# Performance work log

Hardware: AMD Instinct MI355X
Metric: run time of the kernel (lower is better)

The kernel has to match this reference:

```python
import jax, jax.numpy as jnp
import numpy as np

N = 131072      # total nodes
G = 1024        # graphs
NPG = 128       # nodes per graph (equal-sized graphs, batch sorted)
E = 2097152     # edges (avg degree 16)
H = 64          # hidden_channels
K = 30          # sort-pool k
MAXZ = 1000     # max_z
D = 3 * H + 1   # total_latent_dim = hidden*num_layers + 1 = 193
DENSE = ((K - 2) // 2 + 1 - 5 + 1) * 32  # 352


def setup_inputs():
    key = jax.random.key(0)
    ks = jax.random.split(key, 16)
    z = jax.random.randint(ks[0], (N,), 0, MAXZ)
    # within-graph random edges
    g = jax.random.randint(ks[1], (E,), 0, G)
    src = g * NPG + jax.random.randint(ks[2], (E,), 0, NPG)
    dst = g * NPG + jax.random.randint(ks[3], (E,), 0, NPG)
    edge_index = jnp.stack([src, dst])
    batch = jnp.repeat(jnp.arange(G), NPG)

    def w(k, shape, fan):
        return jax.random.normal(k, shape, dtype=jnp.float32) / np.float32(np.sqrt(fan))

    z_table = w(ks[4], (MAXZ, H), H)
    W0 = w(ks[5], (H, H), H); b0 = jnp.zeros((H,), jnp.float32)
    W1 = w(ks[6], (H, H), H); b1 = jnp.zeros((H,), jnp.float32)
    W2 = w(ks[7], (H, H), H); b2 = jnp.zeros((H,), jnp.float32)
    W3 = w(ks[8], (H, 1), H); b3 = jnp.zeros((1,), jnp.float32)
    conv1_w = w(ks[9], (16, D), D); conv1_b = jnp.zeros((16,), jnp.float32)
    conv2_w = w(ks[10], (32, 16, 5), 16 * 5); conv2_b = jnp.zeros((32,), jnp.float32)
    lin1_w = w(ks[11], (DENSE, 128), DENSE); lin1_b = jnp.zeros((128,), jnp.float32)
    lin2_w = w(ks[12], (128, 1), 128); lin2_b = jnp.zeros((1,), jnp.float32)
    return dict(z=z, edge_index=edge_index, batch=batch, z_table=z_table,
                W0=W0, b0=b0, W1=W1, b1=b1, W2=W2, b2=b2, W3=W3, b3=b3,
                conv1_w=conv1_w, conv1_b=conv1_b, conv2_w=conv2_w, conv2_b=conv2_b,
                lin1_w=lin1_w, lin1_b=lin1_b, lin2_w=lin2_w, lin2_b=lin2_b)


def _forward(z, edge_index, z_table, W0, b0, W1, b1, W2, b2, W3, b3,
             conv1_w, conv1_b, conv2_w, conv2_b, lin1_w, lin1_b, lin2_w, lin2_b):
    src, dst = edge_index[0], edge_index[1]
    loop = jnp.arange(N)
    src_sl = jnp.concatenate([src, loop])  # self-loops (gcn_norm)
    dst_sl = jnp.concatenate([dst, loop])
    deg = jax.ops.segment_sum(jnp.ones((E + N,), jnp.float32), dst_sl, num_segments=N)
    dinv = jnp.where(deg > 0, 1.0 / jnp.sqrt(deg), 0.0)
    norm = dinv[src_sl] * dinv[dst_sl]  # sym-normalized edge weights

    def gcn(x, W, b):
        h = x @ W
        agg = jax.ops.segment_sum(h[src_sl] * norm[:, None], dst_sl, num_segments=N)
        return agg + b

    x = z_table[z]  # z_embedding lookup, [N, H]
    xs = []
    for W, b in ((W0, b0), (W1, b1), (W2, b2), (W3, b3)):
        x = jnp.tanh(gcn(x, W, b))
        xs.append(x)
    xc = jnp.concatenate(xs, axis=-1)  # [N, D] (concat of xs[1:])

    # global_sort_pool: sort per graph by last channel (descending), keep top-K.
    xg = xc.reshape(G, NPG, D)
    order = jnp.argsort(-xg[:, :, -1], axis=1)[:, :K]
    topk = jnp.take_along_axis(xg, order[:, :, None], axis=1)  # [G, K, D]

    # conv1: kernel=stride=D over flattened [G, 1, K*D] == per-node linear D->16
    h1 = jax.nn.relu(jnp.einsum('gkd,cd->gck', topk, conv1_w) + conv1_b[None, :, None])  # [G,16,K]
    p = h1.reshape(G, 16, K // 2, 2).max(-1)  # maxpool1d(2,2) -> [G,16,15]
    h2 = jax.nn.relu(
        jax.lax.conv_general_dilated(p, conv2_w, (1,), 'VALID',
                                     dimension_numbers=('NCH', 'OIH', 'NCH'))
        + conv2_b[None, :, None])  # [G,32,11]
    flat = h2.reshape(G, -1)  # channel-major flatten, matches torch .view
    hm = jax.nn.relu(flat @ lin1_w + lin1_b)  # MLP (dropout off in eval)
    return hm @ lin2_w + lin2_b  # [G, 1]


def reference(z, edge_index, batch, z_table, W0, b0, W1, b1, W2, b2, W3, b3,
              conv1_w, conv1_b, conv2_w, conv2_b, lin1_w, lin1_b, lin2_w, lin2_b):
    del batch  # graphs are equal-sized & node ids contiguous: reshape implements sort-pool segmentation
    return _forward(z, edge_index, z_table, W0, b0, W1, b1, W2, b2, W3, b3,
                    conv1_w, conv1_b, conv2_w, conv2_b, lin1_w, lin1_b, lin2_w, lin2_b)
```

## Files before the change

### kernel.cpp

```cpp
#include <hip/hip_runtime.h>

#define NGRAPH  1024
#define E_EDGES 2097152
#define ECAP    2944
#define MAXZ    1000

__device__ __forceinline__ float bfu_lo(unsigned u) { return __uint_as_float(u << 16); }
__device__ __forceinline__ float bfu_hi(unsigned u) { return __uint_as_float(u & 0xFFFF0000u); }
__device__ __forceinline__ unsigned packlo(float f0, float f1) {
    return (__float_as_uint(f0) >> 16) | (__float_as_uint(f1) & 0xFFFF0000u);
}
__device__ __forceinline__ int xh_idx(int r, int k)  { return (r << 6) | (k  ^ ((r & 7) << 3)); }
__device__ __forceinline__ int xl_idx(int r, int k2) { return (r << 5) | (k2 ^ ((r & 7) << 2)); }

__device__ __forceinline__ double tanh_fast(double p) {
    double q = 2.0 * p;
    q = fmin(40.0, fmax(-40.0, q));
    double nf = rint(q * 1.4426950408889634074);
    double r  = fma(nf, -6.93147180369123816490e-01, q);
    r = fma(nf, -1.90821492927058770002e-10, r);
    double er =     2.755731922398589e-07;
    er = fma(er, r, 2.755731922398589e-06);
    er = fma(er, r, 2.4801587301587302e-05);
    er = fma(er, r, 1.984126984126984e-04);
    er = fma(er, r, 1.3888888888888889e-03);
    er = fma(er, r, 8.333333333333333e-03);
    er = fma(er, r, 4.1666666666666664e-02);
    er = fma(er, r, 1.6666666666666666e-01);
    er = fma(er, r, 0.5);
    er = fma(er, r, 1.0);
    er = fma(er, r, 1.0);
    double E = er * __longlong_as_double((long long)(1023 + (int)nf) << 52);
    return 1.0 - 2.0 / (E + 1.0);
}

__global__ void markWS_kernel(float* out) {
    int i = blockIdx.x * 256 + threadIdx.x;
    if (i < NGRAPH) out[i] = 2.0f;
}

__global__ void adjscatter_kernel(const int* __restrict__ ei,
                                  unsigned* __restrict__ adjG) {
    int e = blockIdx.x * 256 + threadIdx.x;
    if (e >= E_EDGES) return;
    int s = ei[e];
    int d = ei[E_EDGES + e];
    int g = s >> 7;
    int sl = s & 127, dl = d & 127;
    atomicAdd(&adjG[((size_t)g << 12) + (dl << 5) + (sl >> 2)], 1u << ((sl & 3) << 3));
}

__global__ __launch_bounds__(1024, 1) void gnn2_kernel(
    const int* __restrict__ z,
    const unsigned* __restrict__ adjG,
    const float* __restrict__ zt,
    const float* __restrict__ W0, const float* __restrict__ b0,
    const float* __restrict__ W1, const float* __restrict__ b1,
    const float* __restrict__ W2, const float* __restrict__ b2,
    const float* __restrict__ W3, const float* __restrict__ b3,
    const float* __restrict__ c1w, const float* __restrict__ c1b,
    const float* __restrict__ c2w, const float* __restrict__ c2b,
    const float* __restrict__ l1w, const float* __restrict__ l1b,
    const float* __restrict__ l2w, const float* __restrict__ l2b,
    float* __restrict__ xdump,
    float* __restrict__ out)
{
    __shared__ __align__(16) float    Xhi[2][8192];
    __shared__ __align__(16) unsigned Xlo[2][4096];
    __shared__ unsigned char  csr[2][ECAP];
    __shared__ unsigned short rp16[2][132];
    __shared__ int            aux[2][128];
    __shared__ int            inv[2][30];
    __shared__ float          kd30f[2][30];
    __shared__ int            w0tot[2];

    const int half = threadIdx.x >> 9;
    const int tt   = threadIdx.x & 511;
    const int g    = (blockIdx.x << 1) | half;
    const int r0 = tt >> 3;
    const int r1 = r0 + 64;
    const int c0 = (tt & 7) << 3;

    float*          XH = Xhi[half];
    unsigned*       XL = Xlo[half];
    unsigned char*  CS = csr[half];
    unsigned short* RP = rp16[half];
    int*            AX = aux[half];

    unsigned* adjM = (unsigned*)XH;

    {
        const uint4* src = (const uint4*)(adjG + ((size_t)g << 12));
        uint4* dst = (uint4*)adjM;
        for (int i = tt; i < 1024; i += 512) dst[i] = src[i];
    }
    if (tt < 30) { inv[half][tt] = tt; kd30f[half][tt] = 0.f; }
    __syncthreads();

    int degv = 0;
    if (tt < 128) {
        for (int w = 0; w < 32; ++w) {
            unsigned u = adjM[(tt << 5) + w];
            degv += (int)((u & 255u) + ((u >> 8) & 255u) + ((u >> 16) & 255u) + (u >> 24));
        }
        AX[tt] = degv;
    }
    if (tt < 128) {
        int v = degv;
        for (int o = 1; o < 64; o <<= 1) {
            int u = __shfl_up(v, o, 64);
            if ((tt & 63) >= o) v += u;
        }
        if (tt == 63) w0tot[half] = v;
        RP[tt + 1] = (unsigned short)v;
    }
    __syncthreads();
    if (tt >= 64 && tt < 128) RP[tt + 1] = (unsigned short)(RP[tt + 1] + w0tot[half]);
    if (tt == 0) RP[0] = 0;
    __syncthreads();

    const int mydeg = (tt < 128) ? AX[tt] : 0;
    const double dv0 = 1.0 / sqrt((double)(AX[r0] + 1));
    const double dv1 = 1.0 / sqrt((double)(AX[r1] + 1));
    const double dvm = 1.0 / sqrt((double)(mydeg + 1));

    if (tt < 128) {
        unsigned pos = RP[tt];
        for (int w = 0; w < 32; ++w) {
            unsigned u = adjM[(tt << 5) + w];
            while (u) {
                int b2 = (u & 0xFFu) ? 0 : (u & 0xFF00u) ? 1 : (u & 0xFF0000u) ? 2 : 3;
                int m = (int)((u >> (b2 << 3)) & 255u);
                unsigned char sv = (unsigned char)((w << 2) + b2);
                for (int q = 0; q < m; ++q) { if (pos < ECAP) CS[pos] = sv; ++pos; }
                u &= ~(0xFFu << (b2 << 3));
            }
        }
    }
    __syncthreads();

    for (int idx = tt; idx < 8192; idx += 512) {
        int n = idx >> 6, c = idx & 63;
        int zv = z[(g << 7) + n];
        zv = (zv < 0) ? 0 : ((zv >= MAXZ) ? MAXZ - 1 : zv);
        XH[xh_idx(n, c)] = zt[zv * 64 + c];
    }
    __syncthreads();

    for (int layer = 0; layer < 3; ++layer) {
        const float* Wg = (layer == 0) ? W0 : (layer == 1) ? W1 : W2;
        const float* bg = (layer == 0) ? b0 : (layer == 1) ? b1 : b2;
        const bool haslo = (layer != 0);

        double accd0[8], accd1[8]; float accf0[8], accf1[8];
#pragma unroll
        for (int j = 0; j < 8; ++j) { accd0[j] = 0.0; accd1[j] = 0.0; accf0[j] = 0.f; accf1[j] = 0.f; }

        for (int k = 0; k < 64; k += 4) {
            float4 a0 = *(const float4*)&XH[xh_idx(r0, k)];
            float4 a1 = *(const float4*)&XH[xh_idx(r1, k)];
            float x0[4] = {a0.x, a0.y, a0.z, a0.w};
            float x1[4] = {a1.x, a1.y, a1.z, a1.w};
            float l0[4], l1[4];
            if (haslo) {
                uint2 u0 = *(const uint2*)&XL[xl_idx(r0, k >> 1)];
                uint2 u1 = *(const uint2*)&XL[xl_idx(r1, k >> 1)];
                l0[0] = bfu_lo(u0.x); l0[1] = bfu_hi(u0.x); l0[2] = bfu_lo(u0.y); l0[3] = bfu_hi(u0.y);
                l1[0] = bfu_lo(u1.x); l1[1] = bfu_hi(u1.x); l1[2] = bfu_lo(u1.y); l1[3] = bfu_hi(u1.y);
            }
#pragma unroll
            for (int kk = 0; kk < 4; ++kk) {
                const float* wr = Wg + ((k + kk) << 6) + c0;
                float4 wa = *(const float4*)wr;
                float4 wb = *(const float4*)(wr + 4);
                float wf[8] = {wa.x, wa.y, wa.z, wa.w, wb.x, wb.y, wb.z, wb.w};
                double xd0 = (double)x0[kk], xd1 = (double)x1[kk];
#pragma unroll
                for (int j = 0; j < 8; ++j) {
                    double wd = (double)wf[j];
                    accd0[j] = fma(xd0, wd, accd0[j]);
                    accd1[j] = fma(xd1, wd, accd1[j]);
                }
                if (haslo) {
#pragma unroll
                    for (int j = 0; j < 8; ++j) {
                        accf0[j] = fmaf(l0[kk], wf[j], accf0[j]);
                        accf1[j] = fmaf(l1[kk], wf[j], accf1[j]);
                    }
                }
            }
        }
        __syncthreads();

        float hfv[2][8], rsv[2][8];
#pragma unroll
        for (int rw = 0; rw < 2; ++rw) {
            int rr = rw ? r1 : r0;
            double dv = rw ? dv1 : dv0;
#pragma unroll
            for (int j = 0; j < 8; ++j) {
                double acc = rw ? (accd1[j] + (double)accf1[j]) : (accd0[j] + (double)accf0[j]);
                double h = dv * acc;
                float hf = (float)h;
                hfv[rw][j] = hf;
                rsv[rw][j] = (float)(h - (double)hf);
            }
            int bi = xh_idx(rr, c0);
            *(float4*)&XH[bi]     = make_float4(hfv[rw][0], hfv[rw][1], hfv[rw][2], hfv[rw][3]);
            *(float4*)&XH[bi + 4] = make_float4(hfv[rw][4], hfv[rw][5], hfv[rw][6], hfv[rw][7]);
            uint4 lv;
            lv.x = packlo(rsv[rw][0], rsv[rw][1]);
            lv.y = packlo(rsv[rw][2], rsv[rw][3]);
            lv.z = packlo(rsv[rw][4], rsv[rw][5]);
            lv.w = packlo(rsv[rw][6], rsv[rw][7]);
            *(uint4*)&XL[xl_idx(rr, c0 >> 1)] = lv;
        }
        __syncthreads();

        double ad[2][8]; float af[2][8];
#pragma unroll
        for (int rw = 0; rw < 2; ++rw)
#pragma unroll
            for (int j = 0; j < 8; ++j) { ad[rw][j] = (double)hfv[rw][j]; af[rw][j] = rsv[rw][j]; }

#pragma unroll
        for (int rw = 0; rw < 2; ++rw) {
            int rr = rw ? r1 : r0;
            for (unsigned e = RP[rr]; e < RP[rr + 1]; ++e) {
                int s = CS[e];
                int bi = (s << 6) | (c0 ^ ((s & 7) << 3));
                float4 a = *(const float4*)&XH[bi];
                float4 b = *(const float4*)&XH[bi + 4];
                uint4 lu = *(const uint4*)&XL[(s << 5) | ((c0 >> 1) ^ ((s & 7) << 2))];
                ad[rw][0] += (double)a.x; ad[rw][1] += (double)a.y;
                ad[rw][2] += (double)a.z; ad[rw][3] += (double)a.w;
                ad[rw][4] += (double)b.x; ad[rw][5] += (double)b.y;
                ad[rw][6] += (double)b.z; ad[rw][7] += (double)b.w;
                af[rw][0] += bfu_lo(lu.x); af[rw][1] += bfu_hi(lu.x);
                af[rw][2] += bfu_lo(lu.y); af[rw][3] += bfu_hi(lu.y);
                af[rw][4] += bfu_lo(lu.z); af[rw][5] += bfu_hi(lu.z);
                af[rw][6] += bfu_lo(lu.w); af[rw][7] += bfu_hi(lu.w);
            }
        }
        __syncthreads();

#pragma unroll
        for (int rw = 0; rw < 2; ++rw) {
            int rr = rw ? r1 : r0;
            double dv = rw ? dv1 : dv0;
            float vf[8], rs[8];
#pragma unroll
            for (int j = 0; j < 8; ++j) {
                double v = tanh_fast(dv * (ad[rw][j] + (double)af[rw][j]) + (double)bg[c0 + j]);
                float vfl = (float)v;
                vf[j] = vfl;
                rs[j] = (float)(v - (double)vfl);
            }
            int bi = xh_idx(rr, c0);
            *(float4*)&XH[bi]     = make_float4(vf[0], vf[1], vf[2], vf[3]);
            *(float4*)&XH[bi + 4] = make_float4(vf[4], vf[5], vf[6], vf[7]);
            uint4 lv;
            lv.x = packlo(rs[0], rs[1]);
            lv.y = packlo(rs[2], rs[3]);
            lv.z = packlo(rs[4], rs[5]);
            lv.w = packlo(rs[6], rs[7]);
            *(uint4*)&XL[xl_idx(rr, c0 >> 1)] = lv;

            if (layer < 2) {
                float* xd = xdump + (((size_t)g * 2 + layer) << 13) + (rr << 6) + c0;
                *(float4*)xd       = make_float4(vf[0], vf[1], vf[2], vf[3]);
                *(float4*)(xd + 4) = make_float4(vf[4], vf[5], vf[6], vf[7]);
            }
        }
        __syncthreads();
    }

    double* h4sD  = (double*)XL;
    double* keydD = ((double*)XL) + 128;

    double sdreg = 0.0;
    if (tt < 128) {
        double sd = 0.0; float sf = 0.f;
        for (int k = 0; k < 64; k += 4) {
            float4 a = *(const float4*)&XH[xh_idx(tt, k)];
            uint2  u = *(const uint2*)&XL[xl_idx(tt, k >> 1)];
            float4 w = *(const float4*)&W3[k];
            sd = fma((double)a.x, (double)w.x, sd);
            sd = fma((double)a.y, (double)w.y, sd);
            sd = fma((double)a.z, (double)w.z, sd);
            sd = fma((double)a.w, (double)w.w, sd);
            sf = fmaf(bfu_lo(u.x), w.x, sf);
            sf = fmaf(bfu_hi(u.x), w.y, sf);
            sf = fmaf(bfu_lo(u.y), w.z, sf);
            sf = fmaf(bfu_hi(u.y), w.w, sf);
        }
        sdreg = sd + (double)sf;
    }
    __syncthreads();
    if (tt < 128) h4sD[tt] = dvm * sdreg;
    __syncthreads();
    double keyreg = 0.0;
    if (tt < 128) {
        double a = h4sD[tt];
        for (unsigned e = RP[tt]; e < RP[tt + 1]; ++e) a += h4sD[CS[e]];
        keyreg = tanh_fast(dvm * a + (double)b3[0]);
        keydD[tt] = keyreg;
    }
    __syncthreads();

    if (tt < 128) {
        int rk = 0;
        for (int j = 0; j < 128; ++j) {
            double kj = keydD[j];
            if (kj > keyreg || (kj == keyreg && j < tt)) ++rk;
        }
        if (rk < 30) { inv[half][rk] = tt; kd30f[half][rk] = (float)keyreg; }
    }
    __syncthreads();

    float* XloF = (float*)XL;
    float* h1v = XloF + 2560;
    float* ppv = XloF + 3040;
    float* flv = XloF + 3280;
    float* hmv = XloF + 3632;

    if (tt < 480) {
        int c = tt & 15, k = tt >> 4;
        int node = inv[half][k];
        const float* wrow = c1w + c * 193;
        const float* xg0 = xdump + ((size_t)g * 2) * 8192 + node * 64;
        const float* xg1 = xg0 + 8192;
        float s8[8];
#pragma unroll
        for (int cg = 0; cg < 8; ++cg) {
            float acc = 0.f;
            float4 xa = *(const float4*)&xg0[cg * 8];
            float4 xb = *(const float4*)&xg0[cg * 8 + 4];
            const float* w0p = wrow + cg * 8;
            acc = fmaf(xa.x, w0p[0], acc); acc = fmaf(xa.y, w0p[1], acc);
            acc = fmaf(xa.z, w0p[2], acc); acc = fmaf(xa.w, w0p[3], acc);
            acc = fmaf(xb.x, w0p[4], acc); acc = fmaf(xb.y, w0p[5], acc);
            acc = fmaf(xb.z, w0p[6], acc); acc = fmaf(xb.w, w0p[7], acc);
            float4 ya = *(const float4*)&xg1[cg * 8];
            float4 yb = *(const float4*)&xg1[cg * 8 + 4];
            const float* w1p = wrow + 64 + cg * 8;
            acc = fmaf(ya.x, w1p[0], acc); acc = fmaf(ya.y, w1p[1], acc);
            acc = fmaf(ya.z, w1p[2], acc); acc = fmaf(ya.w, w1p[3], acc);
            acc = fmaf(yb.x, w1p[4], acc); acc = fmaf(yb.y, w1p[5], acc);
            acc = fmaf(yb.z, w1p[6], acc); acc = fmaf(yb.w, w1p[7], acc);
            const float* w2p = wrow + 128 + cg * 8;
#pragma unroll
            for (int j = 0; j < 8; ++j)
                acc = fmaf(XH[xh_idx(node, cg * 8 + j)], w2p[j], acc);
            s8[cg] = acc;
        }
        float A0 = s8[0] + s8[1], A1 = s8[2] + s8[3];
        float A2 = s8[4] + s8[5], A3 = s8[6] + s8[7];
        float G = (A0 + A1) + (A2 + A3);
        float s = G + c1w[c * 193 + 192] * kd30f[half][k] + c1b[c];
        h1v[c * 30 + k] = s > 0.f ? s : 0.f;
    }
    __syncthreads();
    if (tt < 240) {
        int c = tt & 15, i = tt >> 4;
        float a = h1v[c * 30 + 2 * i], b = h1v[c * 30 + 2 * i + 1];
        ppv[c * 15 + i] = a > b ? a : b;
    }
    __syncthreads();
    if (tt < 352) {
        int o = tt / 11, j = tt % 11;
        float s = c2b[o];
        for (int i = 0; i < 16; ++i)
#pragma unroll
            for (int u = 0; u < 5; ++u)
                s = fmaf(ppv[i * 15 + j + u], c2w[o * 80 + i * 5 + u], s);
        flv[tt] = s > 0.f ? s : 0.f;
    }
    __syncthreads();
    if (tt < 128) {
        float s = l1b[tt];
        for (int i = 0; i < 352; ++i) s = fmaf(flv[i], l1w[i * 128 + tt], s);
        hmv[tt] = s > 0.f ? s : 0.f;
    }
    __syncthreads();
    if (tt < 64) {
        float v = fmaf(hmv[tt], l2w[tt], hmv[tt + 64] * l2w[tt + 64]);
#pragma unroll
        for (int o = 32; o > 0; o >>= 1) v += __shfl_down(v, o, 64);
        if (tt == 0) out[g] = v + l2b[0];
    }
}

__global__ __launch_bounds__(512, 2) void gnn_kernel(
    const int* __restrict__ z,
    const unsigned* __restrict__ adjG,
    const float* __restrict__ zt,
    const float* __restrict__ W0, const float* __restrict__ b0,
    const float* __restrict__ W1, const float* __restrict__ b1,
    const float* __restrict__ W2, const float* __restrict__ b2,
    const float* __restrict__ W3, const float* __restrict__ b3,
    const float* __restrict__ c1w, const float* __restrict__ c1b,
    const float* __restrict__ c2w, const float* __restrict__ c2b,
    const float* __restrict__ l1w, const float* __restrict__ l1b,
    const float* __restrict__ l2w, const float* __restrict__ l2b,
    float* __restrict__ out)
{
    __shared__ __align__(16) float    Xhi[8192];
    __shared__ __align__(16) unsigned Xlo[4096];
    __shared__ unsigned char  csr[ECAP];
    __shared__ unsigned short rp16[132];
    __shared__ int            aux[128];
    __shared__ int            inv[30];
    __shared__ float          kd30f[30];
    __shared__ int            w0tot;

    const int g  = blockIdx.x;
    const int t  = threadIdx.x;
    const int r0 = t >> 3;
    const int r1 = r0 + 64;
    const int c0 = (t & 7) << 3;

    unsigned* adjM = (unsigned*)Xhi;

    {
        const uint4* src = (const uint4*)(adjG + ((size_t)g << 12));
        uint4* dst = (uint4*)adjM;
        for (int i = t; i < 1024; i += 512) dst[i] = src[i];
    }
    if (t < 30) { inv[t] = t; kd30f[t] = 0.f; }
    __syncthreads();

    int degv = 0;
    if (t < 128) {
        for (int w = 0; w < 32; ++w) {
            unsigned u = adjM[(t << 5) + w];
            degv += (int)((u & 255u) + ((u >> 8) & 255u) + ((u >> 16) & 255u) + (u >> 24));
        }
        aux[t] = degv;
    }
    if (t < 128) {
        int v = degv;
        for (int o = 1; o < 64; o <<= 1) {
            int u = __shfl_up(v, o, 64);
            if ((t & 63) >= o) v += u;
        }
        if (t == 63) w0tot = v;
        rp16[t + 1] = (unsigned short)v;
    }
    __syncthreads();
    if (t >= 64 && t < 128) rp16[t + 1] = (unsigned short)(rp16[t + 1] + w0tot);
    if (t == 0) rp16[0] = 0;
    __syncthreads();

    const int mydeg = (t < 128) ? aux[t] : 0;
    const double dv0 = 1.0 / sqrt((double)(aux[r0] + 1));
    const double dv1 = 1.0 / sqrt((double)(aux[r1] + 1));
    const double dvm = 1.0 / sqrt((double)(mydeg + 1));

    if (t < 128) {
        unsigned pos = rp16[t];
        for (int w = 0; w < 32; ++w) {
            unsigned u = adjM[(t << 5) + w];
            while (u) {
                int b2 = (u & 0xFFu) ? 0 : (u & 0xFF00u) ? 1 : (u & 0xFF0000u) ? 2 : 3;
                int m = (int)((u >> (b2 << 3)) & 255u);
                unsigned char sv = (unsigned char)((w << 2) + b2);
                for (int q = 0; q < m; ++q) { if (pos < ECAP) csr[pos] = sv; ++pos; }
                u &= ~(0xFFu << (b2 << 3));
            }
        }
    }
    __syncthreads();

// ... 122 lines not shown
            }
            int bi = xh_idx(rr, c0);
            *(float4*)&Xhi[bi]     = make_float4(vf[0], vf[1], vf[2], vf[3]);
            *(float4*)&Xhi[bi + 4] = make_float4(vf[4], vf[5], vf[6], vf[7]);
            uint4 lv;
            lv.x = packlo(rs[0], rs[1]);
            lv.y = packlo(rs[2], rs[3]);
            lv.z = packlo(rs[4], rs[5]);
            lv.w = packlo(rs[6], rs[7]);
            *(uint4*)&Xlo[xl_idx(rr, c0 >> 1)] = lv;

            const float* w1base = c1w + layer * 64 + c0;
            for (int c = 0; c < 16; ++c) {
                const float* wr = w1base + c * 193;
#pragma unroll
                for (int j = 0; j < 8; ++j)
                    g1p[rw][c] = fmaf(vf[j], wr[j], g1p[rw][c]);
            }
        }
        __syncthreads();
    }

    double* h4sD  = (double*)Xlo;
    double* keydD = ((double*)Xlo) + 128;

    double sdreg = 0.0;
    if (t < 128) {
        double sd = 0.0; float sf = 0.f;
        for (int k = 0; k < 64; k += 4) {
            float4 a = *(const float4*)&Xhi[xh_idx(t, k)];
            uint2  u = *(const uint2*)&Xlo[xl_idx(t, k >> 1)];
            float4 w = *(const float4*)&W3[k];
            sd = fma((double)a.x, (double)w.x, sd);
            sd = fma((double)a.y, (double)w.y, sd);
            sd = fma((double)a.z, (double)w.z, sd);
            sd = fma((double)a.w, (double)w.w, sd);
            sf = fmaf(bfu_lo(u.x), w.x, sf);
            sf = fmaf(bfu_hi(u.x), w.y, sf);
            sf = fmaf(bfu_lo(u.y), w.z, sf);
            sf = fmaf(bfu_hi(u.y), w.w, sf);
        }
        sdreg = sd + (double)sf;
    }
    __syncthreads();
    if (t < 128) h4sD[t] = dvm * sdreg;
    __syncthreads();
    double keyreg = 0.0;
    if (t < 128) {
        double a = h4sD[t];
        for (unsigned e = rp16[t]; e < rp16[t + 1]; ++e) a += h4sD[csr[e]];
        keyreg = tanh_fast(dvm * a + (double)b3[0]);
        keydD[t] = keyreg;
    }
    __syncthreads();

    if (t < 128) {
        int rk = 0;
        for (int j = 0; j < 128; ++j) {
            double kj = keydD[j];
            if (kj > keyreg || (kj == keyreg && j < t)) ++rk;
        }
        if (rk < 30) { inv[rk] = t; kd30f[rk] = (float)keyreg; }
    }

#pragma unroll
    for (int m = 1; m <= 4; m <<= 1) {
#pragma unroll
        for (int rw = 0; rw < 2; ++rw)
#pragma unroll
            for (int c = 0; c < 16; ++c)
                g1p[rw][c] += __shfl_xor(g1p[rw][c], m, 64);
    }
    __syncthreads();
    float* XloF = (float*)Xlo;
    float* G1   = XloF + 512;
    if ((t & 7) == 0) {
#pragma unroll
        for (int c = 0; c < 16; c += 4) {
            *(float4*)&G1[r0 * 16 + c] = make_float4(g1p[0][c], g1p[0][c + 1], g1p[0][c + 2], g1p[0][c + 3]);
            *(float4*)&G1[r1 * 16 + c] = make_float4(g1p[1][c], g1p[1][c + 1], g1p[1][c + 2], g1p[1][c + 3]);
        }
    }
    __syncthreads();

    float* h1v = XloF + 2560;
    float* ppv = XloF + 3040;
    float* flv = XloF + 3280;
    float* hmv = XloF + 3632;

    if (t < 480) {
        int c = t & 15, k = t >> 4;
        int node = inv[k];
        float s = G1[node * 16 + c] + c1w[c * 193 + 192] * kd30f[k] + c1b[c];
        h1v[c * 30 + k] = s > 0.f ? s : 0.f;
    }
    __syncthreads();
    if (t < 240) {
        int c = t & 15, i = t >> 4;
        float a = h1v[c * 30 + 2 * i], b = h1v[c * 30 + 2 * i + 1];
        ppv[c * 15 + i] = a > b ? a : b;
    }
    __syncthreads();
    if (t < 352) {
        int o = t / 11, j = t % 11;
        float s = c2b[o];
        for (int i = 0; i < 16; ++i)
#pragma unroll
            for (int u = 0; u < 5; ++u)
                s = fmaf(ppv[i * 15 + j + u], c2w[o * 80 + i * 5 + u], s);
        flv[t] = s > 0.f ? s : 0.f;
    }
    __syncthreads();
    if (t < 128) {
        float s = l1b[t];
        for (int i = 0; i < 352; ++i) s = fmaf(flv[i], l1w[i * 128 + t], s);
        hmv[t] = s > 0.f ? s : 0.f;
    }
    __syncthreads();
    if (t < 64) {
        float v = fmaf(hmv[t], l2w[t], hmv[t + 64] * l2w[t + 64]);
#pragma unroll
        for (int o = 32; o > 0; o >>= 1) v += __shfl_down(v, o, 64);
        if (t == 0) out[g] = v + l2b[0];
    }
}


extern "C" void kernel_launch(void* const* d_in, const int* in_sizes, int n_in,
                              void* d_out, int out_size, void* d_ws, size_t ws_size,
                              hipStream_t stream) {
    const int*   z   = (const int*)d_in[0];
    const int*   ei  = (const int*)d_in[1];
    const float* zt  = (const float*)d_in[3];
    const float* W0  = (const float*)d_in[4];
    const float* b0  = (const float*)d_in[5];
    const float* W1  = (const float*)d_in[6];
    const float* b1  = (const float*)d_in[7];
    const float* W2  = (const float*)d_in[8];
    const float* b2  = (const float*)d_in[9];
    const float* W3  = (const float*)d_in[10];
    const float* b3  = (const float*)d_in[11];
    const float* c1w = (const float*)d_in[12];
    const float* c1b = (const float*)d_in[13];
    const float* c2w = (const float*)d_in[14];
    const float* c2b = (const float*)d_in[15];
    const float* l1w = (const float*)d_in[16];
    const float* l1b = (const float*)d_in[17];
    const float* l2w = (const float*)d_in[18];
    const float* l2b = (const float*)d_in[19];
    float* out = (float*)d_out;

    const size_t ADJ_B = (size_t)NGRAPH * 4096 * 4;
    const size_t XD_B  = (size_t)NGRAPH * 2 * 8192 * 4;
    if (ws_size < ADJ_B) {
        markWS_kernel<<<4, 256, 0, stream>>>(out);
        return;
    }

    unsigned* adjG = (unsigned*)d_ws;

    hipMemsetAsync(adjG, 0, ADJ_B, stream);
    adjscatter_kernel<<<(E_EDGES + 255) / 256, 256, 0, stream>>>(ei, adjG);

    if (ws_size >= ADJ_B + XD_B) {
        float* xdump = (float*)((char*)d_ws + ADJ_B);
        gnn2_kernel<<<NGRAPH / 2, 1024, 0, stream>>>(z, adjG, zt,
                                                     W0, b0, W1, b1, W2, b2, W3, b3,
                                                     c1w, c1b, c2w, c2b, l1w, l1b, l2w, l2b,
                                                     xdump, out);
    } else {
        gnn_kernel<<<NGRAPH, 512, 0, stream>>>(z, adjG, zt,
                                               W0, b0, W1, b1, W2, b2, W3, b3,
                                               c1w, c1b, c2w, c2b, l1w, l1b, l2w, l2b,
                                               out);
    }
}
```

Measured before the change: 599.7 us.

## Use FP64 MFMA for per-layer dense transform with runtime correctness probe

```diff
diff --git a/kernel.cpp b/kernel.cpp
--- a/kernel.cpp
+++ b/kernel.cpp
@@ -4,6 +4,17 @@
 #define E_EDGES 2097152
 #define ECAP    2944
 #define MAXZ    1000
+
+#if defined(__has_builtin)
+#  if __has_builtin(__builtin_amdgcn_mfma_f64_16x16x4f64)
+#    define HAVE_MFMA64 1
+#  endif
+#endif
+#ifndef HAVE_MFMA64
+#  define HAVE_MFMA64 0
+#endif
+
+typedef __attribute__((ext_vector_type(4))) double double4v;
 
 __device__ __forceinline__ float bfu_lo(unsigned u) { return __uint_as_float(u << 16); }
 __device__ __forceinline__ float bfu_hi(unsigned u) { return __uint_as_float(u & 0xFFFF0000u); }
@@ -50,6 +61,32 @@
     atomicAdd(&adjG[((size_t)g << 12) + (dl << 5) + (sl >> 2)], 1u << ((sl & 3) << 3));
 }
 
+__global__ void mfmaprobe_kernel(int* flag) {
+#if HAVE_MFMA64
+    int l = threadIdx.x;
+    int i16 = l & 15, kq = l >> 4;
+    double A = (double)(i16 * 17 + kq * 3 + 1);
+    double B = (double)(kq * 7 + i16 * 29 + 2);
+    double4v acc = {0.0, 0.0, 0.0, 0.0};
+    acc = __builtin_amdgcn_mfma_f64_16x16x4f64(A, B, acc, 0, 0, 0);
+    bool ok = true;
+#pragma unroll
+    for (int v = 0; v < 4; ++v) {
+        int i = (kq << 2) + v;
+        int j = i16;
+        double ref = 0.0;
+#pragma unroll
+        for (int k = 0; k < 4; ++k)
+            ref += (double)(i * 17 + k * 3 + 1) * (double)(k * 7 + j * 29 + 2);
+        ok = ok && (acc[v] == ref);
+    }
+    unsigned long long m = __ballot(ok);
+    if (l == 0) flag[0] = (m == 0xFFFFFFFFFFFFFFFFull) ? 1 : 0;
+#else
+    if (threadIdx.x == 0) flag[0] = 0;
+#endif
+}
+
 __global__ __launch_bounds__(1024, 1) void gnn2_kernel(
     const int* __restrict__ z,
     const unsigned* __restrict__ adjG,
@@ -62,6 +99,7 @@
     const float* __restrict__ c2w, const float* __restrict__ c2b,
     const float* __restrict__ l1w, const float* __restrict__ l1b,
     const float* __restrict__ l2w, const float* __restrict__ l2b,
+    const int* __restrict__ mfmaflag,
     float* __restrict__ xdump,
     float* __restrict__ out)
 {
@@ -87,6 +125,10 @@
     unsigned short* RP = rp16[half];
     int*            AX = aux[half];
 
+#if HAVE_MFMA64
+    const bool use_mfma = (mfmaflag[0] != 0);
+#endif
+
     unsigned* adjM = (unsigned*)XH;
 
     {
@@ -152,124 +194,247 @@
         const float* bg = (layer == 0) ? b0 : (layer == 1) ? b1 : b2;
         const bool haslo = (layer != 0);
 
-        double accd0[8], accd1[8]; float accf0[8], accf1[8];
-#pragma unroll
-        for (int j = 0; j < 8; ++j) { accd0[j] = 0.0; accd1[j] = 0.0; accf0[j] = 0.f; accf1[j] = 0.f; }
-
-        for (int k = 0; k < 64; k += 4) {
-            float4 a0 = *(const float4*)&XH[xh_idx(r0, k)];
-            float4 a1 = *(const float4*)&XH[xh_idx(r1, k)];
-            float x0[4] = {a0.x, a0.y, a0.z, a0.w};
-            float x1[4] = {a1.x, a1.y, a1.z, a1.w};
-            float l0[4], l1[4];
-            if (haslo) {
-                uint2 u0 = *(const uint2*)&XL[xl_idx(r0, k >> 1)];
-                uint2 u1 = *(const uint2*)&XL[xl_idx(r1, k >> 1)];
-                l0[0] = bfu_lo(u0.x); l0[1] = bfu_hi(u0.x); l0[2] = bfu_lo(u0.y); l0[3] = bfu_hi(u0.y);
-                l1[0] = bfu_lo(u1.x); l1[1] = bfu_hi(u1.x); l1[2] = bfu_lo(u1.y); l1[3] = bfu_hi(u1.y);
-            }
-#pragma unroll
-            for (int kk = 0; kk < 4; ++kk) {
-                const float* wr = Wg + ((k + kk) << 6) + c0;
-                float4 wa = *(const float4*)wr;
-                float4 wb = *(const float4*)(wr + 4);
-                float wf[8] = {wa.x, wa.y, wa.z, wa.w, wb.x, wb.y, wb.z, wb.w};
-                double xd0 = (double)x0[kk], xd1 = (double)x1[kk];
+#if HAVE_MFMA64
+        if (use_mfma) {
+            const int lane = tt & 63;
+            const int wv   = tt >> 6;
+            const int rowbase = wv << 4;
+            const int arow = rowbase + (lane & 15);
+            const int kq   = lane >> 4;
+            double4v acc0 = {0.0, 0.0, 0.0, 0.0};
+            double4v acc1 = {0.0, 0.0, 0.0, 0.0};
+            double4v acc2 = {0.0, 0.0, 0.0, 0.0};
+            double4v acc3 = {0.0, 0.0, 0.0, 0.0};
+            for (int ks = 0; ks < 16; ++ks) {
+                int k = (ks << 2) + kq;
+                double x = (double)XH[xh_idx(arow, k)];
+                if (haslo) {
+                    unsigned u = XL[xl_idx(arow, k >> 1)];
+                    x += (double)((k & 1) ? bfu_hi(u) : bfu_lo(u));
+                }
+                const float* wrk = Wg + (k << 6) + (lane & 15);
+                acc0 = __builtin_amdgcn_mfma_f64_16x16x4f64(x, (double)wrk[0],  acc0, 0, 0, 0);
+                acc1 = __builtin_amdgcn_mfma_f64_16x16x4f64(x, (double)wrk[16], acc1, 0, 0, 0);
+                acc2 = __builtin_amdgcn_mfma_f64_16x16x4f64(x, (double)wrk[32], acc2, 0, 0, 0);
+                acc3 = __builtin_amdgcn_mfma_f64_16x16x4f64(x, (double)wrk[48], acc3, 0, 0, 0);
+            }
+            __syncthreads();
+
+            double dvv[4];
+#pragma unroll
+            for (int v = 0; v < 4; ++v)
+                dvv[v] = 1.0 / sqrt((double)(AX[rowbase + (kq << 2) + v] + 1));
+
+#define STORE_TILE(ACC, T4)                                                       \
+            {                                                                     \
+                int ocol = ((T4) << 4) + (lane & 15);                             \
+                _Pragma("unroll")                                                 \
+                for (int v = 0; v < 4; ++v) {                                     \
+                    int orow = rowbase + (kq << 2) + v;                           \
+                    double h = dvv[v] * (ACC)[v];                                 \
+                    float hf = (float)h;                                          \
+                    float rs = (float)(h - (double)hf);                           \
+                    XH[xh_idx(orow, ocol)] = hf;                                  \
+                    float rsp = __shfl_xor(rs, 1, 64);                            \
+                    if (!(lane & 1))                                              \
+                        XL[xl_idx(orow, ocol >> 1)] = packlo(rs, rsp);            \
+                }                                                                 \
+            }
+            STORE_TILE(acc0, 0)
+            STORE_TILE(acc1, 1)
+            STORE_TILE(acc2, 2)
+            STORE_TILE(acc3, 3)
+#undef STORE_TILE
+            __syncthreads();
+
+            double ad[2][8]; float af[2][8];
+#pragma unroll
+            for (int rw = 0; rw < 2; ++rw) {
+                int rr = rw ? r1 : r0;
+                int bio = xh_idx(rr, c0);
+                float4 h0 = *(const float4*)&XH[bio];
+                float4 h1 = *(const float4*)&XH[bio + 4];
+                uint4  lo = *(const uint4*)&XL[xl_idx(rr, c0 >> 1)];
+                ad[rw][0] = (double)h0.x; ad[rw][1] = (double)h0.y;
+                ad[rw][2] = (double)h0.z; ad[rw][3] = (double)h0.w;
+                ad[rw][4] = (double)h1.x; ad[rw][5] = (double)h1.y;
+                ad[rw][6] = (double)h1.z; ad[rw][7] = (double)h1.w;
+                af[rw][0] = bfu_lo(lo.x); af[rw][1] = bfu_hi(lo.x);
+                af[rw][2] = bfu_lo(lo.y); af[rw][3] = bfu_hi(lo.y);
+                af[rw][4] = bfu_lo(lo.z); af[rw][5] = bfu_hi(lo.z);
+                af[rw][6] = bfu_lo(lo.w); af[rw][7] = bfu_hi(lo.w);
+            }
+#pragma unroll
+            for (int rw = 0; rw < 2; ++rw) {
+                int rr = rw ? r1 : r0;
+                for (unsigned e = RP[rr]; e < RP[rr + 1]; ++e) {
+                    int s = CS[e];
+                    int bi = (s << 6) | (c0 ^ ((s & 7) << 3));
+                    float4 a = *(const float4*)&XH[bi];
+                    float4 b = *(const float4*)&XH[bi + 4];
+                    uint4 lu = *(const uint4*)&XL[(s << 5) | ((c0 >> 1) ^ ((s & 7) << 2))];
+                    ad[rw][0] += (double)a.x; ad[rw][1] += (double)a.y;
+                    ad[rw][2] += (double)a.z; ad[rw][3] += (double)a.w;
+                    ad[rw][4] += (double)b.x; ad[rw][5] += (double)b.y;
+                    ad[rw][6] += (double)b.z; ad[rw][7] += (double)b.w;
+                    af[rw][0] += bfu_lo(lu.x); af[rw][1] += bfu_hi(lu.x);
+                    af[rw][2] += bfu_lo(lu.y); af[rw][3] += bfu_hi(lu.y);
+                    af[rw][4] += bfu_lo(lu.z); af[rw][5] += bfu_hi(lu.z);
+                    af[rw][6] += bfu_lo(lu.w); af[rw][7] += bfu_hi(lu.w);
+                }
+            }
+            __syncthreads();
+
+#pragma unroll
+            for (int rw = 0; rw < 2; ++rw) {
+                int rr = rw ? r1 : r0;
+                double dv = rw ? dv1 : dv0;
+                float vf[8], rs2[8];
 #pragma unroll
                 for (int j = 0; j < 8; ++j) {
-                    double wd = (double)wf[j];
-                    accd0[j] = fma(xd0, wd, accd0[j]);
-                    accd1[j] = fma(xd1, wd, accd1[j]);
-                }
+                    double v = tanh_fast(dv * (ad[rw][j] + (double)af[rw][j]) + (double)bg[c0 + j]);
+                    float vfl = (float)v;
+                    vf[j] = vfl;
+                    rs2[j] = (float)(v - (double)vfl);
+                }
+                int bi = xh_idx(rr, c0);
+                *(float4*)&XH[bi]     = make_float4(vf[0], vf[1], vf[2], vf[3]);
+                *(float4*)&XH[bi + 4] = make_float4(vf[4], vf[5], vf[6], vf[7]);
+                uint4 lv;
+                lv.x = packlo(rs2[0], rs2[1]);
+                lv.y = packlo(rs2[2], rs2[3]);
+                lv.z = packlo(rs2[4], rs2[5]);
+                lv.w = packlo(rs2[6], rs2[7]);
+                *(uint4*)&XL[xl_idx(rr, c0 >> 1)] = lv;
+
+                if (layer < 2) {
+                    float* xd = xdump + (((size_t)g * 2 + layer) << 13) + (rr << 6) + c0;
+                    *(float4*)xd       = make_float4(vf[0], vf[1], vf[2], vf[3]);
+                    *(float4*)(xd + 4) = make_float4(vf[4], vf[5], vf[6], vf[7]);
+                }
+            }
+        } else
+#endif
+        {
+            double accd0[8], accd1[8]; float accf0[8], accf1[8];
+#pragma unroll
+            for (int j = 0; j < 8; ++j) { accd0[j] = 0.0; accd1[j] = 0.0; accf0[j] = 0.f; accf1[j] = 0.f; }
+
+            for (int k = 0; k < 64; k += 4) {
+                float4 a0 = *(const float4*)&XH[xh_idx(r0, k)];
+                float4 a1 = *(const float4*)&XH[xh_idx(r1, k)];
+                float x0[4] = {a0.x, a0.y, a0.z, a0.w};
+                float x1[4] = {a1.x, a1.y, a1.z, a1.w};
+                float l0[4], l1[4];
                 if (haslo) {
+                    uint2 u0 = *(const uint2*)&XL[xl_idx(r0, k >> 1)];
+                    uint2 u1 = *(const uint2*)&XL[xl_idx(r1, k >> 1)];
+                    l0[0] = bfu_lo(u0.x); l0[1] = bfu_hi(u0.x); l0[2] = bfu_lo(u0.y); l0[3] = bfu_hi(u0.y);
+                    l1[0] = bfu_lo(u1.x); l1[1] = bfu_hi(u1.x); l1[2] = bfu_lo(u1.y); l1[3] = bfu_hi(u1.y);
+                }
+#pragma unroll
+                for (int kk = 0; kk < 4; ++kk) {
+                    const float* wr = Wg + ((k + kk) << 6) + c0;
+                    float4 wa = *(const float4*)wr;
+                    float4 wb = *(const float4*)(wr + 4);
+                    float wf[8] = {wa.x, wa.y, wa.z, wa.w, wb.x, wb.y, wb.z, wb.w};
+                    double xd0 = (double)x0[kk], xd1 = (double)x1[kk];
 #pragma unroll
                     for (int j = 0; j < 8; ++j) {
-                        accf0[j] = fmaf(l0[kk], wf[j], accf0[j]);
-                        accf1[j] = fmaf(l1[kk], wf[j], accf1[j]);
+                        double wd = (double)wf[j];
+                        accd0[j] = fma(xd0, wd, accd0[j]);
+                        accd1[j] = fma(xd1, wd, accd1[j]);
                     }
-                }
-            }
-        }
-        __syncthreads();
-
-        float hfv[2][8], rsv[2][8];
-#pragma unroll
-        for (int rw = 0; rw < 2; ++rw) {
-            int rr = rw ? r1 : r0;
-            double dv = rw ? dv1 : dv0;
-#pragma unroll
-            for (int j = 0; j < 8; ++j) {
-                double acc = rw ? (accd1[j] + (double)accf1[j]) : (accd0[j] + (double)accf0[j]);
-                double h = dv * acc;
-                float hf = (float)h;
-                hfv[rw][j] = hf;
-                rsv[rw][j] = (float)(h - (double)hf);
-            }
-            int bi = xh_idx(rr, c0);
-            *(float4*)&XH[bi]     = make_float4(hfv[rw][0], hfv[rw][1], hfv[rw][2], hfv[rw][3]);
-            *(float4*)&XH[bi + 4] = make_float4(hfv[rw][4], hfv[rw][5], hfv[rw][6], hfv[rw][7]);
-            uint4 lv;
-            lv.x = packlo(rsv[rw][0], rsv[rw][1]);
-            lv.y = packlo(rsv[rw][2], rsv[rw][3]);
-            lv.z = packlo(rsv[rw][4], rsv[rw][5]);
-            lv.w = packlo(rsv[rw][6], rsv[rw][7]);
-            *(uint4*)&XL[xl_idx(rr, c0 >> 1)] = lv;
-        }
-        __syncthreads();
-
-        double ad[2][8]; float af[2][8];
-#pragma unroll
-        for (int rw = 0; rw < 2; ++rw)
-#pragma unroll
-            for (int j = 0; j < 8; ++j) { ad[rw][j] = (double)hfv[rw][j]; af[rw][j] = rsv[rw][j]; }
-
-#pragma unroll
-        for (int rw = 0; rw < 2; ++rw) {
-            int rr = rw ? r1 : r0;
-            for (unsigned e = RP[rr]; e < RP[rr + 1]; ++e) {
-                int s = CS[e];
-                int bi = (s << 6) | (c0 ^ ((s & 7) << 3));
-                float4 a = *(const float4*)&XH[bi];
-                float4 b = *(const float4*)&XH[bi + 4];
-                uint4 lu = *(const uint4*)&XL[(s << 5) | ((c0 >> 1) ^ ((s & 7) << 2))];
-                ad[rw][0] += (double)a.x; ad[rw][1] += (double)a.y;
-                ad[rw][2] += (double)a.z; ad[rw][3] += (double)a.w;
-                ad[rw][4] += (double)b.x; ad[rw][5] += (double)b.y;
-                ad[rw][6] += (double)b.z; ad[rw][7] += (double)b.w;
-                af[rw][0] += bfu_lo(lu.x); af[rw][1] += bfu_hi(lu.x);
-                af[rw][2] += bfu_lo(lu.y); af[rw][3] += bfu_hi(lu.y);
-                af[rw][4] += bfu_lo(lu.z); af[rw][5] += bfu_hi(lu.z);
-                af[rw][6] += bfu_lo(lu.w); af[rw][7] += bfu_hi(lu.w);
-            }
-        }
-        __syncthreads();
-
-#pragma unroll
-        for (int rw = 0; rw < 2; ++rw) {
-            int rr = rw ? r1 : r0;
-            double dv = rw ? dv1 : dv0;
-            float vf[8], rs[8];
-#pragma unroll
-            for (int j = 0; j < 8; ++j) {
-                double v = tanh_fast(dv * (ad[rw][j] + (double)af[rw][j]) + (double)bg[c0 + j]);
-                float vfl = (float)v;
-                vf[j] = vfl;
-                rs[j] = (float)(v - (double)vfl);
-            }
-            int bi = xh_idx(rr, c0);
-            *(float4*)&XH[bi]     = make_float4(vf[0], vf[1], vf[2], vf[3]);
-            *(float4*)&XH[bi + 4] = make_float4(vf[4], vf[5], vf[6], vf[7]);
-            uint4 lv;
-            lv.x = packlo(rs[0], rs[1]);
-            lv.y = packlo(rs[2], rs[3]);
-            lv.z = packlo(rs[4], rs[5]);
-            lv.w = packlo(rs[6], rs[7]);
-            *(uint4*)&XL[xl_idx(rr, c0 >> 1)] = lv;
-
-            if (layer < 2) {
-                float* xd = xdump + (((size_t)g * 2 + layer) << 13) + (rr << 6) + c0;
-                *(float4*)xd       = make_float4(vf[0], vf[1], vf[2], vf[3]);
-                *(float4*)(xd + 4) = make_float4(vf[4], vf[5], vf[6], vf[7]);
+                    if (haslo) {
+#pragma unroll
+                        for (int j = 0; j < 8; ++j) {
+                            accf0[j] = fmaf(l0[kk], wf[j], accf0[j]);
+                            accf1[j] = fmaf(l1[kk], wf[j], accf1[j]);
+                        }
+                    }
+                }
+            }
+            __syncthreads();
+
+            float hfv[2][8], rsv[2][8];
+#pragma unroll
+            for (int rw = 0; rw < 2; ++rw) {
+                int rr = rw ? r1 : r0;
+                double dv = rw ? dv1 : dv0;
+#pragma unroll
+                for (int j = 0; j < 8; ++j) {
+                    double acc = rw ? (accd1[j] + (double)accf1[j]) : (accd0[j] + (double)accf0[j]);
+                    double h = dv * acc;
+                    float hf = (float)h;
+                    hfv[rw][j] = hf;
+                    rsv[rw][j] = (float)(h - (double)hf);
+                }
+                int bi = xh_idx(rr, c0);
+                *(float4*)&XH[bi]     = make_float4(hfv[rw][0], hfv[rw][1], hfv[rw][2], hfv[rw][3]);
+                *(float4*)&XH[bi + 4] = make_float4(hfv[rw][4], hfv[rw][5], hfv[rw][6], hfv[rw][7]);
+                uint4 lv;
+                lv.x = packlo(rsv[rw][0], rsv[rw][1]);
+                lv.y = packlo(rsv[rw][2], rsv[rw][3]);
+                lv.z = packlo(rsv[rw][4], rsv[rw][5]);
+                lv.w = packlo(rsv[rw][6], rsv[rw][7]);
+                *(uint4*)&XL[xl_idx(rr, c0 >> 1)] = lv;
+            }
+            __syncthreads();
+
+            double ad[2][8]; float af[2][8];
+#pragma unroll
+            for (int rw = 0; rw < 2; ++rw)
+#pragma unroll
+                for (int j = 0; j < 8; ++j) { ad[rw][j] = (double)hfv[rw][j]; af[rw][j] = rsv[rw][j]; }
+
+#pragma unroll
+            for (int rw = 0; rw < 2; ++rw) {
+                int rr = rw ? r1 : r0;
+                for (unsigned e = RP[rr]; e < RP[rr + 1]; ++e) {
+                    int s = CS[e];
+                    int bi = (s << 6) | (c0 ^ ((s & 7) << 3));
+                    float4 a = *(const float4*)&XH[bi];
+                    float4 b = *(const float4*)&XH[bi + 4];
+                    uint4 lu = *(const uint4*)&XL[(s << 5) | ((c0 >> 1) ^ ((s & 7) << 2))];
+                    ad[rw][0] += (double)a.x; ad[rw][1] += (double)a.y;
+                    ad[rw][2] += (double)a.z; ad[rw][3] += (double)a.w;
+                    ad[rw][4] += (double)b.x; ad[rw][5] += (double)b.y;
+                    ad[rw][6] += (double)b.z; ad[rw][7] += (double)b.w;
+                    af[rw][0] += bfu_lo(lu.x); af[rw][1] += bfu_hi(lu.x);
+                    af[rw][2] += bfu_lo(lu.y); af[rw][3] += bfu_hi(lu.y);
+                    af[rw][4] += bfu_lo(lu.z); af[rw][5] += bfu_hi(lu.z);
+                    af[rw][6] += bfu_lo(lu.w); af[rw][7] += bfu_hi(lu.w);
+                }
+            }
+            __syncthreads();
+
+#pragma unroll
+            for (int rw = 0; rw < 2; ++rw) {
+                int rr = rw ? r1 : r0;
+                double dv = rw ? dv1 : dv0;
+                float vf[8], rs[8];
+#pragma unroll
+                for (int j = 0; j < 8; ++j) {
+                    double v = tanh_fast(dv * (ad[rw][j] + (double)af[rw][j]) + (double)bg[c0 + j]);
+                    float vfl = (float)v;
+                    vf[j] = vfl;
+                    rs[j] = (float)(v - (double)vfl);
+                }
+                int bi = xh_idx(rr, c0);
+                *(float4*)&XH[bi]     = make_float4(vf[0], vf[1], vf[2], vf[3]);
+                *(float4*)&XH[bi + 4] = make_float4(vf[4], vf[5], vf[6], vf[7]);
+                uint4 lv;
+                lv.x = packlo(rs[0], rs[1]);
+                lv.y = packlo(rs[2], rs[3]);
+                lv.z = packlo(rs[4], rs[5]);
+                lv.w = packlo(rs[6], rs[7]);
+                *(uint4*)&XL[xl_idx(rr, c0 >> 1)] = lv;
+
+                if (layer < 2) {
+                    float* xd = xdump + (((size_t)g * 2 + layer) << 13) + (rr << 6) + c0;
+                    *(float4*)xd       = make_float4(vf[0], vf[1], vf[2], vf[3]);
+                    *(float4*)(xd + 4) = make_float4(vf[4], vf[5], vf[6], vf[7]);
+                }
             }
         }
         __syncthreads();
@@ -747,6 +912,7 @@
 
     const size_t ADJ_B = (size_t)NGRAPH * 4096 * 4;
     const size_t XD_B  = (size_t)NGRAPH * 2 * 8192 * 4;
+    const size_t FL_B  = 256;
     if (ws_size < ADJ_B) {
         markWS_kernel<<<4, 256, 0, stream>>>(out);
         return;
@@ -757,12 +923,14 @@
     hipMemsetAsync(adjG, 0, ADJ_B, stream);
     adjscatter_kernel<<<(E_EDGES + 255) / 256, 256, 0, stream>>>(ei, adjG);
 
-    if (ws_size >= ADJ_B + XD_B) {
+    if (ws_size >= ADJ_B + XD_B + FL_B) {
         float* xdump = (float*)((char*)d_ws + ADJ_B);
+        int*   flag  = (int*)((char*)d_ws + ADJ_B + XD_B);
+        mfmaprobe_kernel<<<1, 64, 0, stream>>>(flag);
         gnn2_kernel<<<NGRAPH / 2, 1024, 0, stream>>>(z, adjG, zt,
                                                      W0, b0, W1, b1, W2, b2, W3, b3,
                                                      c1w, c1b, c2w, c2b, l1w, l1b, l2w, l2b,
-                                                     xdump, out);
+                                                     flag, xdump, out);
     } else {
         gnn_kernel<<<NGRAPH, 512, 0, stream>>>(z, adjG, zt,
                                                W0, b0, W1, b1, W2, b2, W3, b3,
```

Result: slower. 652.0 us (+8.7%).

## Balance aggregation work by degree-sorted row pairing and store fp32 residuals

Applied to the files above, without the earlier changes.

```diff
diff --git a/kernel.cpp b/kernel.cpp
--- a/kernel.cpp
+++ b/kernel.cpp
@@ -66,10 +66,11 @@
     float* __restrict__ out)
 {
     __shared__ __align__(16) float    Xhi[2][8192];
-    __shared__ __align__(16) unsigned Xlo[2][4096];
+    __shared__ __align__(16) float    Xlo[2][8192];
     __shared__ unsigned char  csr[2][ECAP];
     __shared__ unsigned short rp16[2][132];
     __shared__ int            aux[2][128];
+    __shared__ unsigned char  perm[2][128];
     __shared__ int            inv[2][30];
     __shared__ float          kd30f[2][30];
     __shared__ int            w0tot[2];
@@ -77,12 +78,10 @@
     const int half = threadIdx.x >> 9;
     const int tt   = threadIdx.x & 511;
     const int g    = (blockIdx.x << 1) | half;
-    const int r0 = tt >> 3;
-    const int r1 = r0 + 64;
     const int c0 = (tt & 7) << 3;
 
     float*          XH = Xhi[half];
-    unsigned*       XL = Xlo[half];
+    float*          XL = Xlo[half];
     unsigned char*  CS = csr[half];
     unsigned short* RP = rp16[half];
     int*            AX = aux[half];
@@ -120,8 +119,6 @@
     __syncthreads();
 
     const int mydeg = (tt < 128) ? AX[tt] : 0;
-    const double dv0 = 1.0 / sqrt((double)(AX[r0] + 1));
-    const double dv1 = 1.0 / sqrt((double)(AX[r1] + 1));
     const double dvm = 1.0 / sqrt((double)(mydeg + 1));
 
     if (tt < 128) {
@@ -137,7 +134,22 @@
             }
         }
     }
-    __syncthreads();
+    if (tt < 128) {
+        int dmine = AX[tt];
+        int rk = 0;
+        for (int j = 0; j < 128; ++j) {
+            int dj = AX[j];
+            if (dj > dmine || (dj == dmine && j < tt)) ++rk;
+        }
+        perm[half][rk] = (unsigned char)tt;
+    }
+    __syncthreads();
+
+    const int q    = tt >> 3;
+    const int rowA = perm[half][q];
+    const int rowB = perm[half][127 - q];
+    const double dvA = 1.0 / sqrt((double)(AX[rowA] + 1));
+    const double dvB = 1.0 / sqrt((double)(AX[rowB] + 1));
 
     for (int idx = tt; idx < 8192; idx += 512) {
         int n = idx >> 6, c = idx & 63;
@@ -157,16 +169,16 @@
         for (int j = 0; j < 8; ++j) { accd0[j] = 0.0; accd1[j] = 0.0; accf0[j] = 0.f; accf1[j] = 0.f; }
 
         for (int k = 0; k < 64; k += 4) {
-            float4 a0 = *(const float4*)&XH[xh_idx(r0, k)];
-            float4 a1 = *(const float4*)&XH[xh_idx(r1, k)];
+            float4 a0 = *(const float4*)&XH[xh_idx(rowA, k)];
+            float4 a1 = *(const float4*)&XH[xh_idx(rowB, k)];
             float x0[4] = {a0.x, a0.y, a0.z, a0.w};
             float x1[4] = {a1.x, a1.y, a1.z, a1.w};
             float l0[4], l1[4];
             if (haslo) {
-                uint2 u0 = *(const uint2*)&XL[xl_idx(r0, k >> 1)];
-                uint2 u1 = *(const uint2*)&XL[xl_idx(r1, k >> 1)];
-                l0[0] = bfu_lo(u0.x); l0[1] = bfu_hi(u0.x); l0[2] = bfu_lo(u0.y); l0[3] = bfu_hi(u0.y);
-                l1[0] = bfu_lo(u1.x); l1[1] = bfu_hi(u1.x); l1[2] = bfu_lo(u1.y); l1[3] = bfu_hi(u1.y);
+                float4 u0 = *(const float4*)&XL[xh_idx(rowA, k)];
+                float4 u1 = *(const float4*)&XL[xh_idx(rowB, k)];
+                l0[0] = u0.x; l0[1] = u0.y; l0[2] = u0.z; l0[3] = u0.w;
+                l1[0] = u1.x; l1[1] = u1.y; l1[2] = u1.z; l1[3] = u1.w;
             }
 #pragma unroll
             for (int kk = 0; kk < 4; ++kk) {
@@ -195,8 +207,8 @@
         float hfv[2][8], rsv[2][8];
 #pragma unroll
         for (int rw = 0; rw < 2; ++rw) {
-            int rr = rw ? r1 : r0;
-            double dv = rw ? dv1 : dv0;
+            int rr = rw ? rowB : rowA;
+            double dv = rw ? dvB : dvA;
 #pragma unroll
             for (int j = 0; j < 8; ++j) {
                 double acc = rw ? (accd1[j] + (double)accf1[j]) : (accd0[j] + (double)accf0[j]);
@@ -208,12 +220,8 @@
             int bi = xh_idx(rr, c0);
             *(float4*)&XH[bi]     = make_float4(hfv[rw][0], hfv[rw][1], hfv[rw][2], hfv[rw][3]);
             *(float4*)&XH[bi + 4] = make_float4(hfv[rw][4], hfv[rw][5], hfv[rw][6], hfv[rw][7]);
-            uint4 lv;
-            lv.x = packlo(rsv[rw][0], rsv[rw][1]);
-            lv.y = packlo(rsv[rw][2], rsv[rw][3]);
-            lv.z = packlo(rsv[rw][4], rsv[rw][5]);
-            lv.w = packlo(rsv[rw][6], rsv[rw][7]);
-            *(uint4*)&XL[xl_idx(rr, c0 >> 1)] = lv;
+            *(float4*)&XL[bi]     = make_float4(rsv[rw][0], rsv[rw][1], rsv[rw][2], rsv[rw][3]);
+            *(float4*)&XL[bi + 4] = make_float4(rsv[rw][4], rsv[rw][5], rsv[rw][6], rsv[rw][7]);
         }
         __syncthreads();
 
@@ -225,46 +233,43 @@
 
 #pragma unroll
         for (int rw = 0; rw < 2; ++rw) {
-            int rr = rw ? r1 : r0;
+            int rr = rw ? rowB : rowA;
             for (unsigned e = RP[rr]; e < RP[rr + 1]; ++e) {
                 int s = CS[e];
                 int bi = (s << 6) | (c0 ^ ((s & 7) << 3));
-                float4 a = *(const float4*)&XH[bi];
-                float4 b = *(const float4*)&XH[bi + 4];
-                uint4 lu = *(const uint4*)&XL[(s << 5) | ((c0 >> 1) ^ ((s & 7) << 2))];
+                float4 a  = *(const float4*)&XH[bi];
+                float4 b  = *(const float4*)&XH[bi + 4];
+                float4 la = *(const float4*)&XL[bi];
+                float4 lb = *(const float4*)&XL[bi + 4];
                 ad[rw][0] += (double)a.x; ad[rw][1] += (double)a.y;
                 ad[rw][2] += (double)a.z; ad[rw][3] += (double)a.w;
                 ad[rw][4] += (double)b.x; ad[rw][5] += (double)b.y;
                 ad[rw][6] += (double)b.z; ad[rw][7] += (double)b.w;
-                af[rw][0] += bfu_lo(lu.x); af[rw][1] += bfu_hi(lu.x);
-                af[rw][2] += bfu_lo(lu.y); af[rw][3] += bfu_hi(lu.y);
-                af[rw][4] += bfu_lo(lu.z); af[rw][5] += bfu_hi(lu.z);
-                af[rw][6] += bfu_lo(lu.w); af[rw][7] += bfu_hi(lu.w);
+                af[rw][0] += la.x; af[rw][1] += la.y;
+                af[rw][2] += la.z; af[rw][3] += la.w;
+                af[rw][4] += lb.x; af[rw][5] += lb.y;
+                af[rw][6] += lb.z; af[rw][7] += lb.w;
             }
         }
         __syncthreads();
 
 #pragma unroll
         for (int rw = 0; rw < 2; ++rw) {
-            int rr = rw ? r1 : r0;
-            double dv = rw ? dv1 : dv0;
-            float vf[8], rs[8];
+            int rr = rw ? rowB : rowA;
+            double dv = rw ? dvB : dvA;
+            float vf[8], rs2[8];
 #pragma unroll
             for (int j = 0; j < 8; ++j) {
                 double v = tanh_fast(dv * (ad[rw][j] + (double)af[rw][j]) + (double)bg[c0 + j]);
                 float vfl = (float)v;
                 vf[j] = vfl;
-                rs[j] = (float)(v - (double)vfl);
+                rs2[j] = (float)(v - (double)vfl);
             }
             int bi = xh_idx(rr, c0);
             *(float4*)&XH[bi]     = make_float4(vf[0], vf[1], vf[2], vf[3]);
             *(float4*)&XH[bi + 4] = make_float4(vf[4], vf[5], vf[6], vf[7]);
-            uint4 lv;
-            lv.x = packlo(rs[0], rs[1]);
-            lv.y = packlo(rs[2], rs[3]);
-            lv.z = packlo(rs[4], rs[5]);
-            lv.w = packlo(rs[6], rs[7]);
-            *(uint4*)&XL[xl_idx(rr, c0 >> 1)] = lv;
+            *(float4*)&XL[bi]     = make_float4(rs2[0], rs2[1], rs2[2], rs2[3]);
+            *(float4*)&XL[bi + 4] = make_float4(rs2[4], rs2[5], rs2[6], rs2[7]);
 
             if (layer < 2) {
                 float* xd = xdump + (((size_t)g * 2 + layer) << 13) + (rr << 6) + c0;
@@ -283,16 +288,16 @@
         double sd = 0.0; float sf = 0.f;
         for (int k = 0; k < 64; k += 4) {
             float4 a = *(const float4*)&XH[xh_idx(tt, k)];
-            uint2  u = *(const uint2*)&XL[xl_idx(tt, k >> 1)];
+            float4 u = *(const float4*)&XL[xh_idx(tt, k)];
             float4 w = *(const float4*)&W3[k];
             sd = fma((double)a.x, (double)w.x, sd);
             sd = fma((double)a.y, (double)w.y, sd);
             sd = fma((double)a.z, (double)w.z, sd);
             sd = fma((double)a.w, (double)w.w, sd);
-            sf = fmaf(bfu_lo(u.x), w.x, sf);
-            sf = fmaf(bfu_hi(u.x), w.y, sf);
-            sf = fmaf(bfu_lo(u.y), w.z, sf);
-            sf = fmaf(bfu_hi(u.y), w.w, sf);
+            sf = fmaf(u.x, w.x, sf);
+            sf = fmaf(u.y, w.y, sf);
+            sf = fmaf(u.z, w.z, sf);
+            sf = fmaf(u.w, w.w, sf);
         }
         sdreg = sd + (double)sf;
     }
@@ -318,7 +323,7 @@
     }
     __syncthreads();
 
-    float* XloF = (float*)XL;
+    float* XloF = XL;
     float* h1v = XloF + 2560;
     float* ppv = XloF + 3040;
     float* flv = XloF + 3280;
```

Result: faster. 578.0 us (-3.6%).
